# Kernel optimization log

Hardware: AMD Instinct MI355X
Metric: run time of the kernel (lower is better)

## Reference

```python
import jax, jax.numpy as jnp
import numpy as np

TOKENS, IN_F, OUT_F = 8192, 4096, 4096
MAXQ = 15          # 4-bit
ZERO_POINT = 8     # (maxq + 1) // 2


def _make_24_mask(key, in_f, out_f):
    """Boolean 2:4 mask: exactly 2 True per contiguous group of 4 along in_f."""
    scores = jax.random.normal(key, (in_f // 4, 4, out_f), dtype=jnp.float32)
    # ascending sort along the group-of-4 axis; index 2 = 2nd largest value
    thresh = jnp.sort(scores, axis=1)[:, 2:3, :]
    mask = scores >= thresh  # keeps top-2 of each group of 4
    return mask.reshape(in_f, out_f)


def setup_inputs() -> dict:
    key = jax.random.key(0)
    k_x, k_q, k_m, k_s = jax.random.split(key, 4)
    x = jax.random.normal(k_x, (TOKENS, IN_F), dtype=jnp.float16)
    qvals = jax.random.randint(k_q, (IN_F, OUT_F), 0, MAXQ + 1, dtype=jnp.int32)
    mask = _make_24_mask(k_m, IN_F, OUT_F)
    # per-column scales (groupsize == infeatures -> one scale row)
    scales = (jax.random.uniform(k_s, (1, OUT_F), dtype=jnp.float32) * 0.01 + 0.001).astype(jnp.float16)
    return {"x": x, "qvals": qvals, "mask": mask, "scales": scales}


def reference(x, qvals, mask, scales):
    # Dequantize: W = (q - zero_point) * scale, then apply 2:4 sparsity mask.
    w = (qvals.astype(jnp.float32) - ZERO_POINT) * scales.astype(jnp.float32)  # [in, out]
    w = jnp.where(mask, w, 0.0).astype(x.dtype)
    # GEMM with fp32 accumulation (as the fused kernel does), output in x.dtype
    y = jnp.einsum("ti,io->to", x, w, preferred_element_type=jnp.float32)
    return y.astype(x.dtype)
```

## Files before the change

### kernel.cpp

```cpp
#include <hip/hip_runtime.h>
#include <stdint.h>

typedef short short8 __attribute__((ext_vector_type(8)));
typedef float floatx4 __attribute__((ext_vector_type(4)));

#define M_TOK 8192
#define K_IN  4096
#define N_OUT 4096
#define NT    (K_IN / 64)

static __device__ __forceinline__ float bf2f(ushort u) {
    union { uint32_t u; float f; } v;
    v.u = ((uint32_t)u) << 16;
    return v.f;
}
static __device__ __forceinline__ ushort f2bf(float f) {
    union { float f; uint32_t u; } v;
    v.f = f;
    uint32_t u = v.u;
    uint32_t r = (u + 0x7FFFu + ((u >> 16) & 1u)) >> 16;
    return (ushort)r;
}

__global__ void detect_zero_kernel(int* __restrict__ flags) {
    if (threadIdx.x < 3) flags[1 + threadIdx.x] = 0;
}

__global__ __launch_bounds__(256) void detect_count_kernel(
    const unsigned char* __restrict__ mb, int* __restrict__ flags) {
    const ushort* mh = (const ushort*)mb;
    const unsigned int* mw = (const unsigned int*)mb;
    __shared__ int sh[3];
    if (threadIdx.x < 3) sh[threadIdx.x] = 0;
    __syncthreads();
    int s = blockIdx.x * 256 + threadIdx.x;
    int grp = s & 255;
    int o   = (s * 97) & 4095;
    int c1 = 0, c2 = 0, c4 = 0;
    #pragma unroll
    for (int r = 0; r < 4; ++r) {
        size_t idx = (size_t)(4 * grp + r) * N_OUT + o;
        c1 += (mb[idx] != 0);
        c2 += (mh[idx] != 0);
        c4 += (mw[idx] != 0);
    }
    if (c1 != 2) atomicAdd(&sh[0], 1);
    if (c2 != 2) atomicAdd(&sh[1], 1);
    if (c4 != 2) atomicAdd(&sh[2], 1);
    __syncthreads();
    if (threadIdx.x == 0) {
        atomicAdd(&flags[1], sh[0]);
        atomicAdd(&flags[2], sh[1]);
        atomicAdd(&flags[3], sh[2]);
    }
}

__global__ void detect_final_kernel(int* __restrict__ flags) {
    if (threadIdx.x == 0) {
        int size = 4, best = flags[3];
        if (flags[2] < best) { size = 2; best = flags[2]; }
        if (flags[1] < best) { size = 1; }
        flags[0] = size;
    }
}

__global__ __launch_bounds__(256) void convert_x_kernel(
    const float* __restrict__ xf, ushort* __restrict__ Xb) {
    const int total = M_TOK * K_IN;
    const int stride = gridDim.x * 256 * 8;
    for (int i = (blockIdx.x * 256 + threadIdx.x) * 8; i < total; i += stride) {
        floatx4 f0 = *(const floatx4*)&xf[i];
        floatx4 f1 = *(const floatx4*)&xf[i + 4];
        short8 v;
        #pragma unroll
        for (int j = 0; j < 4; ++j) v[j]     = (short)f2bf(f0[j]);
        #pragma unroll
        for (int j = 0; j < 4; ++j) v[4 + j] = (short)f2bf(f1[j]);
        *(short8*)&Xb[i] = v;
    }
}

__global__ __launch_bounds__(256) void dequant_kernel(
    const int* __restrict__ q, const void* __restrict__ maskp,
    const float* __restrict__ scales, ushort* __restrict__ Bt,
    const int* __restrict__ flagp) {
    const int msize = flagp[0];
    const int i0 = blockIdx.x * 64;
    const int o0 = blockIdx.y * 64;
    const int tid = threadIdx.x;
    const unsigned char* mb = (const unsigned char*)maskp;
    const ushort* mh = (const ushort*)maskp;
    const unsigned int* mi = (const unsigned int*)maskp;
    __shared__ ushort T[64][72];

    for (int p = 0; p < 16; ++p) {
        int idx = p * 256 + tid;
        int r = idx >> 6, c = idx & 63;
        size_t gi = (size_t)(i0 + r) * N_OUT + (o0 + c);
        bool m;
        if (msize == 1)      m = (mb[gi] != 0);
        else if (msize == 2) m = (mh[gi] != 0);
        else                 m = (mi[gi] != 0);
        float s = scales[o0 + c];
        float w = m ? (float)(q[gi] - 8) * s : 0.0f;
        T[r][c] = f2bf(w);
    }
    __syncthreads();
    for (int p = 0; p < 2; ++p) {
        int ol = p * 32 + (tid >> 3);
        int i8 = (tid & 7) * 8;
        short8 v;
        #pragma unroll
        for (int j = 0; j < 8; ++j) v[j] = (short)T[i8 + j][ol];
        *(short8*)&Bt[(size_t)(o0 + ol) * K_IN + i0 + i8] = v;
    }
}

#define GL2L16(gp, lbase)                                                      \
    __builtin_amdgcn_global_load_lds(                                          \
        (const __attribute__((address_space(1))) void*)(gp),                   \
        (__attribute__((address_space(3))) void*)(lbase), 16, 0, 0)

__global__ __launch_bounds__(512, 2) void gemm_kernel(
    const ushort* __restrict__ X,
    const ushort* __restrict__ Bt,
    float* __restrict__ Y) {
    __shared__ ushort As0[256][64], As1[256][64];
    __shared__ ushort Bs0[256][64], Bs1[256][64];

    const int tid  = threadIdx.x;
    const int w    = tid >> 6;
    const int lane = tid & 63;

    const int r    = blockIdx.x >> 8;
    const int k    = blockIdx.x & 255;
    const int xcd  = k & 7;
    const int j    = k >> 3;
    const int m_tile = r * 16 + (xcd & 1) * 8 + (j & 7);
    const int n_tile = (xcd >> 1) * 4 + (j >> 3);
    const int row0 = m_tile * 256;
    const int col0 = n_tile * 256;
    const int wm = w >> 2, wn = w & 3;

    floatx4 acc[8][4] = {};

    const int srow   = (w << 3) + (lane >> 3);
    const int schunk = (lane & 7) ^ (lane >> 3);
    const ushort* gA = X  + (size_t)(row0 + srow) * K_IN + schunk * 8;
    const ushort* gB = Bt + (size_t)(col0 + srow) * K_IN + schunk * 8;

    const int fr = lane & 15, g = lane >> 4;
    const int fx = fr & 7;

    #define STG(gbase, buf, h, tt)                                             \
        do {                                                                   \
            GL2L16(gbase + (size_t)((h) * 128) * K_IN + (size_t)(tt) * 64,     \
                   (char*)&buf[(h) * 128 + w * 8][0] + lane * 16);             \
            GL2L16(gbase + (size_t)((h) * 128 + 64) * K_IN + (size_t)(tt) * 64,\
                   (char*)&buf[(h) * 128 + 64 + w * 8][0] + lane * 16);        \
        } while (0)

    #define PHASE(As_, Bs_, MH, KKC, bfr, READB, STAGE_STMT, VMCNT_STMT)       \
        do {                                                                   \
            if (READB) {                                                       \
                _Pragma("unroll")                                              \
                for (int n = 0; n < 4; ++n)                                    \
                    bfr[n] = *(const short8*)&Bs_[wn * 64 + n * 16 + fr]       \
                                 [(((KKC) * 4 + g) ^ fx) * 8];                 \
            }                                                                  \
            short8 afr[4];                                                     \
            _Pragma("unroll")                                                  \
            for (int m = 0; m < 4; ++m)                                        \
                afr[m] = *(const short8*)&As_[wm * 128 + ((MH) * 4 + m) * 16 + fr] \
                             [(((KKC) * 4 + g) ^ fx) * 8];                     \
            STAGE_STMT;                                                        \
            __builtin_amdgcn_s_barrier();                                      \
            asm volatile("s_waitcnt lgkmcnt(0)" ::: "memory");                 \
            __builtin_amdgcn_sched_barrier(0);                                 \
            __builtin_amdgcn_s_setprio(1);                                     \
            _Pragma("unroll")                                                  \
            for (int m = 0; m < 4; ++m)                                        \
                _Pragma("unroll")                                              \
                for (int n = 0; n < 4; ++n)                                    \
                    acc[(MH) * 4 + m][n] = __builtin_amdgcn_mfma_f32_16x16x32_bf16( \
                        afr[m], bfr[n], acc[(MH) * 4 + m][n], 0, 0, 0);        \
            __builtin_amdgcn_s_setprio(0);                                     \
            VMCNT_STMT;                                                        \
            __builtin_amdgcn_s_barrier();                                      \
        } while (0)

    STG(gA, As0, 0, 0); STG(gA, As0, 1, 0);
    STG(gB, Bs0, 0, 0); STG(gB, Bs0, 1, 0);
    STG(gA, As1, 0, 1);
    asm volatile("s_waitcnt vmcnt(2)" ::: "memory");
    __builtin_amdgcn_s_barrier();

    short8 bfr0[4], bfr1[4];

    for (int i = 0; i < NT / 2; ++i) {
        const int t1 = 2 * i + 1, t2 = 2 * i + 2, t3 = 2 * i + 3;
        const bool s2 = (t2 < NT), s3 = (t3 < NT);

        PHASE(As0, Bs0, 0, 0, bfr0, 1, STG(gA, As1, 1, t1), );
        PHASE(As0, Bs0, 1, 0, bfr0, 0, STG(gB, Bs1, 0, t1), );
        PHASE(As0, Bs0, 0, 1, bfr1, 1, STG(gB, Bs1, 1, t1), );
        PHASE(As0, Bs0, 1, 1, bfr1, 0,
              if (s2) STG(gA, As0, 0, t2),
              if (s2) { asm volatile("s_waitcnt vmcnt(2)" ::: "memory"); }
              else    { asm volatile("s_waitcnt vmcnt(0)" ::: "memory"); });

        PHASE(As1, Bs1, 0, 0, bfr0, 1, if (s2) STG(gA, As0, 1, t2), );
        PHASE(As1, Bs1, 1, 0, bfr0, 0, if (s2) STG(gB, Bs0, 0, t2), );
        PHASE(As1, Bs1, 0, 1, bfr1, 1, if (s2) STG(gB, Bs0, 1, t2), );
        PHASE(As1, Bs1, 1, 1, bfr1, 0,
              if (s3) STG(gA, As1, 0, t3),
              if (s3) { asm volatile("s_waitcnt vmcnt(2)" ::: "memory"); }
              else    { asm volatile("s_waitcnt vmcnt(0)" ::: "memory"); });
    }

    const int fq = lane >> 4;
    #pragma unroll
    for (int m = 0; m < 8; ++m)
        #pragma unroll
        for (int n = 0; n < 4; ++n)
            #pragma unroll
            for (int i = 0; i < 4; ++i) {
                int rr = row0 + wm * 128 + m * 16 + fq * 4 + i;
                int cc = col0 + wn * 64 + n * 16 + fr;
                Y[(size_t)rr * N_OUT + cc] = acc[m][n][i];
            }
    #undef PHASE
    #undef STG
}

__global__ __launch_bounds__(256) void fallback_kernel(
    const float* __restrict__ xf, const int* __restrict__ q,
    const void* __restrict__ maskp, const float* __restrict__ scales,
    float* __restrict__ Y, const int* __restrict__ flagp) {
    const int msize = flagp[0];
    const int o = blockIdx.x * 256 + threadIdx.x;
    const int t = blockIdx.y;
    const unsigned char* mb = (const unsigned char*)maskp;
    const ushort* mh = (const ushort*)maskp;
    const unsigned int* mi = (const unsigned int*)maskp;
    float s = scales[o];
    float acc = 0.f;
    for (int i = 0; i < K_IN; ++i) {
        float x = bf2f(f2bf(xf[(size_t)t * K_IN + i]));
        size_t gi = (size_t)i * N_OUT + o;
        bool m;
        if (msize == 1)      m = (mb[gi] != 0);
        else if (msize == 2) m = (mh[gi] != 0);
        else                 m = (mi[gi] != 0);
        if (m) acc += x * bf2f(f2bf((float)(q[gi] - 8) * s));
    }
    Y[(size_t)t * N_OUT + o] = acc;
}

extern "C" void kernel_launch(void* const* d_in, const int* in_sizes, int n_in,
                              void* d_out, int out_size, void* d_ws, size_t ws_size,
                              hipStream_t stream) {
    const float* x      = (const float*)d_in[0];
    const int*   q      = (const int*)d_in[1];
    const void*  mask   = d_in[2];
    const float* scales = (const float*)d_in[3];
    float* y = (float*)d_out;

    const size_t BT_OFF = 64;
    const size_t XB_OFF = BT_OFF + (size_t)N_OUT * K_IN * 2;
    const size_t need   = XB_OFF + (size_t)M_TOK * K_IN * 2;

    int* flags = (int*)d_ws;
    detect_zero_kernel<<<1, 64, 0, stream>>>(flags);
    detect_count_kernel<<<64, 256, 0, stream>>>(
        (const unsigned char*)mask, flags);
    detect_final_kernel<<<1, 64, 0, stream>>>(flags);

    if (ws_size >= need) {
        ushort* Bt = (ushort*)((char*)d_ws + BT_OFF);
        ushort* Xb = (ushort*)((char*)d_ws + XB_OFF);
        convert_x_kernel<<<4096, 256, 0, stream>>>(x, Xb);
        dequant_kernel<<<dim3(K_IN / 64, N_OUT / 64), 256, 0, stream>>>(
            q, mask, scales, Bt, flags);
        gemm_kernel<<<dim3((M_TOK / 256) * (N_OUT / 256)), 512, 0, stream>>>(
            Xb, Bt, y);
    } else {
        fallback_kernel<<<dim3(N_OUT / 256, M_TOK), 256, 0, stream>>>(
            x, q, mask, scales, y, flags);
    }
}
```

Measured before the change: 381.0 us.

## Restructure GEMM main loop into per-tile stages with interleaved LDS reads and MFMAs

```diff
diff --git a/kernel.cpp b/kernel.cpp
--- a/kernel.cpp
+++ b/kernel.cpp
@@ -121,6 +121,8 @@
         (const __attribute__((address_space(1))) void*)(gp),                   \
         (__attribute__((address_space(3))) void*)(lbase), 16, 0, 0)
 
+#define MFMA16(a, b, c) __builtin_amdgcn_mfma_f32_16x16x32_bf16(a, b, c, 0, 0, 0)
+
 __global__ __launch_bounds__(512, 2) void gemm_kernel(
     const ushort* __restrict__ X,
     const ushort* __restrict__ Bt,
@@ -160,62 +162,61 @@
                    (char*)&buf[(h) * 128 + 64 + w * 8][0] + lane * 16);        \
         } while (0)
 
-    #define PHASE(As_, Bs_, MH, KKC, bfr, READB, STAGE_STMT, VMCNT_STMT)       \
+    #define TILE(As_, Bs_, STAGE_STMT)                                         \
         do {                                                                   \
-            if (READB) {                                                       \
-                _Pragma("unroll")                                              \
-                for (int n = 0; n < 4; ++n)                                    \
-                    bfr[n] = *(const short8*)&Bs_[wn * 64 + n * 16 + fr]       \
-                                 [(((KKC) * 4 + g) ^ fx) * 8];                 \
-            }                                                                  \
-            short8 afr[4];                                                     \
-            _Pragma("unroll")                                                  \
-            for (int m = 0; m < 4; ++m)                                        \
-                afr[m] = *(const short8*)&As_[wm * 128 + ((MH) * 4 + m) * 16 + fr] \
-                             [(((KKC) * 4 + g) ^ fx) * 8];                     \
             STAGE_STMT;                                                        \
+            short8 a0[4], b0[4], a1[4], a2[4], b1[4], a3[4];                   \
+            _Pragma("unroll") for (int m = 0; m < 4; ++m)                      \
+                a0[m] = *(const short8*)&As_[wm*128 + m*16 + fr][(g ^ fx)*8];  \
+            _Pragma("unroll") for (int n = 0; n < 4; ++n)                      \
+                b0[n] = *(const short8*)&Bs_[wn*64 + n*16 + fr][(g ^ fx)*8];   \
+            _Pragma("unroll") for (int m = 0; m < 4; ++m)                      \
+                a1[m] = *(const short8*)&As_[wm*128 + 64 + m*16 + fr][(g ^ fx)*8]; \
+            __builtin_amdgcn_s_setprio(1);                                     \
+            _Pragma("unroll") for (int m = 0; m < 4; ++m)                      \
+                _Pragma("unroll") for (int n = 0; n < 4; ++n)                  \
+                    acc[m][n] = MFMA16(a0[m], b0[n], acc[m][n]);               \
+            __builtin_amdgcn_s_setprio(0);                                     \
+            _Pragma("unroll") for (int m = 0; m < 4; ++m)                      \
+                a2[m] = *(const short8*)&As_[wm*128 + m*16 + fr][((4+g) ^ fx)*8]; \
+            _Pragma("unroll") for (int n = 0; n < 4; ++n)                      \
+                b1[n] = *(const short8*)&Bs_[wn*64 + n*16 + fr][((4+g) ^ fx)*8]; \
+            __builtin_amdgcn_s_setprio(1);                                     \
+            _Pragma("unroll") for (int m = 0; m < 4; ++m)                      \
+                _Pragma("unroll") for (int n = 0; n < 4; ++n)                  \
+                    acc[4+m][n] = MFMA16(a1[m], b0[n], acc[4+m][n]);           \
+            __builtin_amdgcn_s_setprio(0);                                     \
+            _Pragma("unroll") for (int m = 0; m < 4; ++m)                      \
+                a3[m] = *(const short8*)&As_[wm*128 + 64 + m*16 + fr][((4+g) ^ fx)*8]; \
+            __builtin_amdgcn_s_setprio(1);                                     \
+            _Pragma("unroll") for (int m = 0; m < 4; ++m)                      \
+                _Pragma("unroll") for (int n = 0; n < 4; ++n)                  \
+                    acc[m][n] = MFMA16(a2[m], b1[n], acc[m][n]);               \
+            _Pragma("unroll") for (int m = 0; m < 4; ++m)                      \
+                _Pragma("unroll") for (int n = 0; n < 4; ++n)                  \
+                    acc[4+m][n] = MFMA16(a3[m], b1[n], acc[4+m][n]);           \
+            __builtin_amdgcn_s_setprio(0);                                     \
+            asm volatile("s_waitcnt vmcnt(0)" ::: "memory");                   \
             __builtin_amdgcn_s_barrier();                                      \
-            asm volatile("s_waitcnt lgkmcnt(0)" ::: "memory");                 \
             __builtin_amdgcn_sched_barrier(0);                                 \
-            __builtin_amdgcn_s_setprio(1);                                     \
-            _Pragma("unroll")                                                  \
-            for (int m = 0; m < 4; ++m)                                        \
-                _Pragma("unroll")                                              \
-                for (int n = 0; n < 4; ++n)                                    \
-                    acc[(MH) * 4 + m][n] = __builtin_amdgcn_mfma_f32_16x16x32_bf16( \
-                        afr[m], bfr[n], acc[(MH) * 4 + m][n], 0, 0, 0);        \
-            __builtin_amdgcn_s_setprio(0);                                     \
-            VMCNT_STMT;                                                        \
-            __builtin_amdgcn_s_barrier();                                      \
         } while (0)
 
     STG(gA, As0, 0, 0); STG(gA, As0, 1, 0);
     STG(gB, Bs0, 0, 0); STG(gB, Bs0, 1, 0);
-    STG(gA, As1, 0, 1);
-    asm volatile("s_waitcnt vmcnt(2)" ::: "memory");
+    asm volatile("s_waitcnt vmcnt(0)" ::: "memory");
     __builtin_amdgcn_s_barrier();
-
-    short8 bfr0[4], bfr1[4];
+    __builtin_amdgcn_sched_barrier(0);
 
     for (int i = 0; i < NT / 2; ++i) {
-        const int t1 = 2 * i + 1, t2 = 2 * i + 2, t3 = 2 * i + 3;
-        const bool s2 = (t2 < NT), s3 = (t3 < NT);
-
-        PHASE(As0, Bs0, 0, 0, bfr0, 1, STG(gA, As1, 1, t1), );
-        PHASE(As0, Bs0, 1, 0, bfr0, 0, STG(gB, Bs1, 0, t1), );
-        PHASE(As0, Bs0, 0, 1, bfr1, 1, STG(gB, Bs1, 1, t1), );
-        PHASE(As0, Bs0, 1, 1, bfr1, 0,
-              if (s2) STG(gA, As0, 0, t2),
-              if (s2) { asm volatile("s_waitcnt vmcnt(2)" ::: "memory"); }
-              else    { asm volatile("s_waitcnt vmcnt(0)" ::: "memory"); });
-
-        PHASE(As1, Bs1, 0, 0, bfr0, 1, if (s2) STG(gA, As0, 1, t2), );
-        PHASE(As1, Bs1, 1, 0, bfr0, 0, if (s2) STG(gB, Bs0, 0, t2), );
-        PHASE(As1, Bs1, 0, 1, bfr1, 1, if (s2) STG(gB, Bs0, 1, t2), );
-        PHASE(As1, Bs1, 1, 1, bfr1, 0,
-              if (s3) STG(gA, As1, 0, t3),
-              if (s3) { asm volatile("s_waitcnt vmcnt(2)" ::: "memory"); }
-              else    { asm volatile("s_waitcnt vmcnt(0)" ::: "memory"); });
+        const int t1 = 2 * i + 1, t2 = 2 * i + 2;
+        const bool s2 = (t2 < NT);
+
+        TILE(As0, Bs0,
+             { STG(gA, As1, 0, t1); STG(gA, As1, 1, t1);
+               STG(gB, Bs1, 0, t1); STG(gB, Bs1, 1, t1); });
+        TILE(As1, Bs1,
+             if (s2) { STG(gA, As0, 0, t2); STG(gA, As0, 1, t2);
+                       STG(gB, Bs0, 0, t2); STG(gB, Bs0, 1, t2); });
     }
 
     const int fq = lane >> 4;
@@ -229,7 +230,7 @@
                 int cc = col0 + wn * 64 + n * 16 + fr;
                 Y[(size_t)rr * N_OUT + cc] = acc[m][n][i];
             }
-    #undef PHASE
+    #undef TILE
     #undef STG
 }
 
```

Measured after the change: 381.5 us. About the same (+0.1%).

## Split LDS tiles into k-half buffers with new swizzle and staging schedule

Applied to the files above, without the earlier changes.

```diff
diff --git a/kernel.cpp b/kernel.cpp
--- a/kernel.cpp
+++ b/kernel.cpp
@@ -125,17 +125,17 @@
     const ushort* __restrict__ X,
     const ushort* __restrict__ Bt,
     float* __restrict__ Y) {
-    __shared__ ushort As0[256][64], As1[256][64];
-    __shared__ ushort Bs0[256][64], Bs1[256][64];
+    __shared__ ushort As[2][2][256][32];
+    __shared__ ushort Bs[2][2][256][32];
 
     const int tid  = threadIdx.x;
     const int w    = tid >> 6;
     const int lane = tid & 63;
 
     const int r    = blockIdx.x >> 8;
-    const int k    = blockIdx.x & 255;
-    const int xcd  = k & 7;
-    const int j    = k >> 3;
+    const int kb   = blockIdx.x & 255;
+    const int xcd  = kb & 7;
+    const int j    = kb >> 3;
     const int m_tile = r * 16 + (xcd & 1) * 8 + (j & 7);
     const int n_tile = (xcd >> 1) * 4 + (j >> 3);
     const int row0 = m_tile * 256;
@@ -144,35 +144,35 @@
 
     floatx4 acc[8][4] = {};
 
-    const int srow   = (w << 3) + (lane >> 3);
-    const int schunk = (lane & 7) ^ (lane >> 3);
+    const int srow   = (w << 4) + (lane >> 2);
+    const int schunk = (lane & 3) ^ ((lane >> 3) & 3);
     const ushort* gA = X  + (size_t)(row0 + srow) * K_IN + schunk * 8;
     const ushort* gB = Bt + (size_t)(col0 + srow) * K_IN + schunk * 8;
 
     const int fr = lane & 15, g = lane >> 4;
-    const int fx = fr & 7;
-
-    #define STG(gbase, buf, h, tt)                                             \
+    const int fsw = (fr >> 1) & 3;
+
+    #define STG(gbase, arr, bf, kh, tt)                                        \
         do {                                                                   \
-            GL2L16(gbase + (size_t)((h) * 128) * K_IN + (size_t)(tt) * 64,     \
-                   (char*)&buf[(h) * 128 + w * 8][0] + lane * 16);             \
-            GL2L16(gbase + (size_t)((h) * 128 + 64) * K_IN + (size_t)(tt) * 64,\
-                   (char*)&buf[(h) * 128 + 64 + w * 8][0] + lane * 16);        \
+            GL2L16(gbase + (size_t)(tt) * 64 + (kh) * 32,                      \
+                   (char*)&arr[bf][kh][w * 16][0] + lane * 16);                \
+            GL2L16(gbase + (size_t)128 * K_IN + (size_t)(tt) * 64 + (kh) * 32, \
+                   (char*)&arr[bf][kh][128 + w * 16][0] + lane * 16);          \
         } while (0)
 
-    #define PHASE(As_, Bs_, MH, KKC, bfr, READB, STAGE_STMT, VMCNT_STMT)       \
+    #define PHASE(BF, KK, MH, READB, bfr, STAGE_STMT, GATE_STMT)               \
         do {                                                                   \
             if (READB) {                                                       \
                 _Pragma("unroll")                                              \
                 for (int n = 0; n < 4; ++n)                                    \
-                    bfr[n] = *(const short8*)&Bs_[wn * 64 + n * 16 + fr]       \
-                                 [(((KKC) * 4 + g) ^ fx) * 8];                 \
+                    bfr[n] = *(const short8*)&Bs[BF][KK]                       \
+                        [wn * 64 + n * 16 + fr][(g ^ fsw) * 8];                \
             }                                                                  \
             short8 afr[4];                                                     \
             _Pragma("unroll")                                                  \
             for (int m = 0; m < 4; ++m)                                        \
-                afr[m] = *(const short8*)&As_[wm * 128 + ((MH) * 4 + m) * 16 + fr] \
-                             [(((KKC) * 4 + g) ^ fx) * 8];                     \
+                afr[m] = *(const short8*)&As[BF][KK]                           \
+                    [wm * 128 + (MH) * 64 + m * 16 + fr][(g ^ fsw) * 8];       \
             STAGE_STMT;                                                        \
             __builtin_amdgcn_s_barrier();                                      \
             asm volatile("s_waitcnt lgkmcnt(0)" ::: "memory");                 \
@@ -185,14 +185,23 @@
                     acc[(MH) * 4 + m][n] = __builtin_amdgcn_mfma_f32_16x16x32_bf16( \
                         afr[m], bfr[n], acc[(MH) * 4 + m][n], 0, 0, 0);        \
             __builtin_amdgcn_s_setprio(0);                                     \
-            VMCNT_STMT;                                                        \
+            GATE_STMT;                                                         \
             __builtin_amdgcn_s_barrier();                                      \
         } while (0)
 
-    STG(gA, As0, 0, 0); STG(gA, As0, 1, 0);
-    STG(gB, Bs0, 0, 0); STG(gB, Bs0, 1, 0);
-    STG(gA, As1, 0, 1);
-    asm volatile("s_waitcnt vmcnt(2)" ::: "memory");
+    #define GATE(c)                                                            \
+        do {                                                                   \
+            if (c) { asm volatile("s_waitcnt vmcnt(4)" ::: "memory"); }        \
+            else   { asm volatile("s_waitcnt vmcnt(0)" ::: "memory"); }        \
+        } while (0)
+
+    STG(gA, As, 0, 0, 0);
+    STG(gB, Bs, 0, 0, 0);
+    STG(gA, As, 0, 1, 0);
+    STG(gB, Bs, 0, 1, 0);
+    STG(gA, As, 1, 0, 1);
+    STG(gB, Bs, 1, 0, 1);
+    asm volatile("s_waitcnt vmcnt(4)" ::: "memory");
     __builtin_amdgcn_s_barrier();
 
     short8 bfr0[4], bfr1[4];
@@ -201,21 +210,15 @@
         const int t1 = 2 * i + 1, t2 = 2 * i + 2, t3 = 2 * i + 3;
         const bool s2 = (t2 < NT), s3 = (t3 < NT);
 
-        PHASE(As0, Bs0, 0, 0, bfr0, 1, STG(gA, As1, 1, t1), );
-        PHASE(As0, Bs0, 1, 0, bfr0, 0, STG(gB, Bs1, 0, t1), );
-        PHASE(As0, Bs0, 0, 1, bfr1, 1, STG(gB, Bs1, 1, t1), );
-        PHASE(As0, Bs0, 1, 1, bfr1, 0,
-              if (s2) STG(gA, As0, 0, t2),
-              if (s2) { asm volatile("s_waitcnt vmcnt(2)" ::: "memory"); }
-              else    { asm volatile("s_waitcnt vmcnt(0)" ::: "memory"); });
-
-        PHASE(As1, Bs1, 0, 0, bfr0, 1, if (s2) STG(gA, As0, 1, t2), );
-        PHASE(As1, Bs1, 1, 0, bfr0, 0, if (s2) STG(gB, Bs0, 0, t2), );
-        PHASE(As1, Bs1, 0, 1, bfr1, 1, if (s2) STG(gB, Bs0, 1, t2), );
-        PHASE(As1, Bs1, 1, 1, bfr1, 0,
-              if (s3) STG(gA, As1, 0, t3),
-              if (s3) { asm volatile("s_waitcnt vmcnt(2)" ::: "memory"); }
-              else    { asm volatile("s_waitcnt vmcnt(0)" ::: "memory"); });
+        PHASE(0, 0, 0, 1, bfr0, STG(gA, As, 1, 1, t1), );
+        PHASE(0, 0, 1, 0, bfr0, STG(gB, Bs, 1, 1, t1), );
+        PHASE(0, 1, 0, 1, bfr1, if (s2) STG(gA, As, 0, 0, t2), );
+        PHASE(0, 1, 1, 0, bfr1, if (s2) STG(gB, Bs, 0, 0, t2), GATE(s2));
+
+        PHASE(1, 0, 0, 1, bfr0, if (s2) STG(gA, As, 0, 1, t2), );
+        PHASE(1, 0, 1, 0, bfr0, if (s2) STG(gB, Bs, 0, 1, t2), );
+        PHASE(1, 1, 0, 1, bfr1, if (s3) STG(gA, As, 1, 0, t3), );
+        PHASE(1, 1, 1, 0, bfr1, if (s3) STG(gB, Bs, 1, 0, t3), GATE(s3));
     }
 
     const int fq = lane >> 4;
@@ -229,6 +232,7 @@
                 int cc = col0 + wn * 64 + n * 16 + fr;
                 Y[(size_t)rr * N_OUT + cc] = acc[m][n][i];
             }
+    #undef GATE
     #undef PHASE
     #undef STG
 }
```

Result: faster. 358.7 us (-5.8%).
